# Performance work log

Measured on AMD Instinct MI355X. Metric: run time of the kernel, lower is better.

## Reference

```python
import jax, jax.numpy as jnp
import numpy as np

NUM_HEADS = 8

def _feature_map(t):
    return jax.nn.elu(t) + 1.0

def setup_inputs() -> dict:
    key = jax.random.key(0)
    ks = jax.random.split(key, 7)
    B, S, D = 2, 1024, 512
    sc = 1.0 / np.sqrt(D)
    return {
        'x':  jax.random.normal(ks[0], (B, S, D), dtype=jnp.float32),
        'Wq': jax.random.normal(ks[1], (D, D), dtype=jnp.float32) * sc,
        'Wk': jax.random.normal(ks[2], (D, D), dtype=jnp.float32) * sc,
        'Wv': jax.random.normal(ks[3], (D, D), dtype=jnp.float32) * sc,
        'Wo': jax.random.normal(ks[4], (D, D), dtype=jnp.float32) * sc,
        'bo': jnp.zeros((D,), dtype=jnp.float32),
        'Wg': jax.random.normal(ks[5], (2 * D, D), dtype=jnp.float32) * (1.0 / np.sqrt(2 * D)),
        'bg': jnp.zeros((D,), dtype=jnp.float32),
    }

def reference(x, Wq, Wk, Wv, Wo, bo, Wg, bg):
    B, S, D = x.shape
    H = NUM_HEADS
    hd = D // H
    # projections, split heads -> [B,S,H,hd]
    q = _feature_map((x @ Wq).reshape(B, S, H, hd))
    k = _feature_map((x @ Wk).reshape(B, S, H, hd))
    v = (x @ Wv).reshape(B, S, H, hd)
    # causal linear attention via cumulative sums
    kv = jnp.einsum('bshd,bshe->bshde', k, v)        # [B,S,H,hd,hd]
    kv_cumsum = jnp.cumsum(kv, axis=1)
    k_cumsum = jnp.cumsum(k, axis=1)
    numerator = jnp.einsum('bshd,bshde->bshe', q, kv_cumsum)
    denominator = jnp.einsum('bshd,bshd->bsh', q, k_cumsum)[..., None]
    out = (numerator / (denominator + 1e-6)).reshape(B, S, D)
    out = out @ Wo + bo
    gate = jax.nn.sigmoid(jnp.concatenate([x, out], axis=-1) @ Wg + bg)
    return x + gate * (out - x)
```

## Files before the change

### kernel.cpp

```cpp
#include <hip/hip_runtime.h>
#include <hip/hip_bf16.h>
#include <math.h>


typedef __bf16 bf16x8 __attribute__((ext_vector_type(8)));
typedef __bf16 bf16x4 __attribute__((ext_vector_type(4)));
typedef float f32x4 __attribute__((ext_vector_type(4)));

#define MFMA16(a, b, c) __builtin_amdgcn_mfma_f32_16x16x32_bf16(a, b, c, 0, 0, 0)

__device__ __forceinline__ float elu1(float v) { return v > 0.f ? v + 1.f : __expf(v); }

__device__ __forceinline__ void gload16(const void* g, void* l) {
    __builtin_amdgcn_global_load_lds((const __attribute__((address_space(1))) void*)g,
                                     (__attribute__((address_space(3))) void*)l, 16, 0, 0);
}

__global__ __launch_bounds__(256) void prep_kernel(
    const float* __restrict__ x, const float* __restrict__ Wq, const float* __restrict__ Wk,
    const float* __restrict__ Wv, const float* __restrict__ Wo, const float* __restrict__ Wg,
    __bf16* __restrict__ xb, __bf16* __restrict__ wqkvT, __bf16* __restrict__ woT,
    __bf16* __restrict__ wgT) {
    int z = blockIdx.z;
    if (z == 5) {
        int bid = blockIdx.y * 16 + blockIdx.x;
        int base = (bid * 256 + threadIdx.x) * 8;
        bf16x8 o;
#pragma unroll
        for (int j = 0; j < 8; j++) o[j] = (__bf16)x[base + j];
        *(bf16x8*)&xb[base] = o;
        return;
    }
    const float* in;
    __bf16* out;
    int R = 512, C = 512;
    if (z == 0) { in = Wq; out = wqkvT; }
    else if (z == 1) { in = Wk; out = wqkvT + (size_t)512 * 512; }
    else if (z == 2) { in = Wv; out = wqkvT + (size_t)1024 * 512; }
    else if (z == 3) { in = Wo; out = woT; }
    else { in = Wg; out = wgT; R = 1024; }
    if ((int)blockIdx.y * 32 >= R) return;
    __shared__ float t[32][33];
    int bx = blockIdx.x, by = blockIdx.y;
    int tx = threadIdx.x & 31, ty = threadIdx.x >> 5;
#pragma unroll
    for (int i = 0; i < 32; i += 8)
        t[ty + i][tx] = in[(size_t)(by * 32 + ty + i) * C + bx * 32 + tx];
    __syncthreads();
#pragma unroll
    for (int i = 0; i < 32; i += 8)
        out[(size_t)(bx * 32 + ty + i) * R + by * 32 + tx] = (__bf16)t[tx][ty + i];
}

template <int MODE, int BM, int BN>
__global__ __launch_bounds__(256) void gemm_kernel(
    const __bf16* __restrict__ A, const __bf16* __restrict__ A2,
    const __bf16* __restrict__ Bw, const float* __restrict__ bias,
    const float* __restrict__ xf, const float* __restrict__ proj,
    float* __restrict__ outf, __bf16* __restrict__ outb,
    __bf16* __restrict__ q_out, __bf16* __restrict__ k_out,
    __bf16* __restrict__ kt_out, __bf16* __restrict__ vt_out, int K) {
    constexpr int MI = BM / 32, NI = BN / 32;
    constexpr int LA = BM / 64, LB = BN / 64;
    constexpr int L = LA + LB;
    __shared__ __bf16 sA[3 * BM * 32];
    __shared__ __bf16 sB[3 * BN * 32];
    int bm = blockIdx.x, bn = blockIdx.y;
    int tid = threadIdx.x, w = tid >> 6, l = tid & 63;
    int wr = (w >> 1) * (16 * MI), wc = (w & 1) * (16 * NI);
    int r = tid >> 2, c = (tid & 3) * 8;
    f32x4 acc[MI][NI] = {};
    const int nt = K / 32;

    auto stage = [&](int t, int buf) {
        int k0 = t * 32;
        const __bf16* a0 = A;
        int gka = k0, lda = K;
        if (MODE == 2) {
            lda = 512;
            if (k0 >= 512) { a0 = A2; gka = k0 - 512; }
        }
#pragma unroll
        for (int i = 0; i < LA; i++)
            gload16(&a0[(size_t)(bm * BM + i * 64 + r) * lda + gka + c],
                    &sA[buf * (BM * 32) + i * 2048 + w * 512]);
#pragma unroll
        for (int i = 0; i < LB; i++)
            gload16(&Bw[(size_t)(bn * BN + i * 64 + r) * K + k0 + c],
                    &sB[buf * (BN * 32) + i * 2048 + w * 512]);
    };

    stage(0, 0);
    stage(1, 1);
    for (int t = 0; t < nt; t++) {
        if (t + 1 < nt) {
            if constexpr (L == 2) asm volatile("s_waitcnt vmcnt(2)" ::: "memory");
            else asm volatile("s_waitcnt vmcnt(3)" ::: "memory");
        } else {
            asm volatile("s_waitcnt vmcnt(0)" ::: "memory");
        }
        asm volatile("s_barrier" ::: "memory");
        if (t + 2 < nt) stage(t + 2, (t + 2) % 3);
        int buf = t % 3;
        bf16x8 af[MI], bfr[NI];
#pragma unroll
        for (int mi = 0; mi < MI; mi++)
            af[mi] = *(const bf16x8*)&sA[buf * (BM * 32) + (wr + mi * 16 + (l & 15)) * 32 + ((l >> 4) << 3)];
#pragma unroll
        for (int ni = 0; ni < NI; ni++)
            bfr[ni] = *(const bf16x8*)&sB[buf * (BN * 32) + (wc + ni * 16 + (l & 15)) * 32 + ((l >> 4) << 3)];
#pragma unroll
        for (int mi = 0; mi < MI; mi++)
#pragma unroll
            for (int ni = 0; ni < NI; ni++)
                acc[mi][ni] = MFMA16(af[mi], bfr[ni], acc[mi][ni]);
    }

    if (MODE == 0) {
#pragma unroll
        for (int mi = 0; mi < MI; mi++) {
            int gm0 = bm * BM + wr + mi * 16 + ((l >> 4) << 2);
            int b = gm0 >> 10, s0 = gm0 & 1023;
#pragma unroll
            for (int ni = 0; ni < NI; ni++) {
                int gn = bn * BN + wc + ni * 16 + (l & 15);
                int which = gn >> 9, h = (gn >> 6) & 7, d = gn & 63;
                int bh = b * 8 + h;
                if (which == 0) {
#pragma unroll
                    for (int j = 0; j < 4; j++)
                        q_out[((size_t)(bh * 1024 + s0 + j)) * 64 + d] = (__bf16)elu1(acc[mi][ni][j]);
                } else if (which == 1) {
                    bf16x4 pk;
#pragma unroll
                    for (int j = 0; j < 4; j++) {
                        __bf16 tb = (__bf16)elu1(acc[mi][ni][j]);
                        pk[j] = tb;
                        k_out[((size_t)(bh * 1024 + s0 + j)) * 64 + d] = tb;
                    }
                    *(bf16x4*)&kt_out[((size_t)(bh * 64 + d)) * 1024 + s0] = pk;
                } else {
                    bf16x4 pv;
#pragma unroll
                    for (int j = 0; j < 4; j++) pv[j] = (__bf16)acc[mi][ni][j];
                    *(bf16x4*)&vt_out[((size_t)(bh * 64 + d)) * 1024 + s0] = pv;
                }
            }
        }
    } else {
#pragma unroll
        for (int mi = 0; mi < MI; mi++)
#pragma unroll
            for (int ni = 0; ni < NI; ni++)
#pragma unroll
                for (int j = 0; j < 4; j++) {
                    int gm = bm * BM + wr + mi * 16 + ((l >> 4) << 2) + j;
                    int gn = bn * BN + wc + ni * 16 + (l & 15);
                    float v = acc[mi][ni][j] + bias[gn];
                    if (MODE == 1) {
                        outf[(size_t)gm * 512 + gn] = v;
                        outb[(size_t)gm * 512 + gn] = (__bf16)v;
                    } else {
                        float g = 1.f / (1.f + __expf(-v));
                        float xv = xf[(size_t)gm * 512 + gn];
                        float pv = proj[(size_t)gm * 512 + gn];
                        outf[(size_t)gm * 512 + gn] = xv + g * (pv - xv);
                    }
                }
    }
}

__global__ __launch_bounds__(256) void mc_kernel(const __bf16* __restrict__ ktb,
                                                 const __bf16* __restrict__ vtb,
                                                 float* __restrict__ Mc, float* __restrict__ ksc) {
    int blk = blockIdx.x;
    int bh = blk >> 3, ch = blk & 7;
    int tid = threadIdx.x, w = tid >> 6, l = tid & 63;
    const __bf16* vb = vtb + (size_t)bh * 65536 + ch * 128;
    const __bf16* kp = ktb + (size_t)bh * 65536 + ch * 128;
    f32x4 macc[4] = {};
#pragma unroll
    for (int ks = 0; ks < 4; ks++) {
        bf16x8 a = *(const bf16x8*)&vb[(size_t)(w * 16 + (l & 15)) * 1024 + ks * 32 + ((l >> 4) << 3)];
#pragma unroll
        for (int ni = 0; ni < 4; ni++) {
            bf16x8 bb = *(const bf16x8*)&kp[(size_t)(ni * 16 + (l & 15)) * 1024 + ks * 32 + ((l >> 4) << 3)];
            macc[ni] = MFMA16(a, bb, macc[ni]);
        }
    }
    float* mout = Mc + (size_t)blk * 4096;
#pragma unroll
    for (int ni = 0; ni < 4; ni++)
#pragma unroll
        for (int j = 0; j < 4; j++)
            mout[(size_t)(w * 16 + ((l >> 4) << 2) + j) * 64 + ni * 16 + (l & 15)] = macc[ni][j];
    if (tid < 64) {
        float s = 0.f;
        const __bf16* kr = ktb + (size_t)(bh * 64 + tid) * 1024 + ch * 128;
#pragma unroll
        for (int t = 0; t < 16; t++) {
            bf16x8 v = *(const bf16x8*)&kr[t * 8];
#pragma unroll
            for (int j = 0; j < 8; j++) s += (float)v[j];
        }
        ksc[blk * 64 + tid] = s;
    }
}

__global__ __launch_bounds__(256) void attn_chunk_kernel(
    const __bf16* __restrict__ qb, const __bf16* __restrict__ kb,
    const __bf16* __restrict__ vtb, const float* __restrict__ Mc,
    const float* __restrict__ ksc, __bf16* __restrict__ attn_out) {
    int blk = blockIdx.x;
    int bh = blk >> 3, ch = blk & 7;
    int b = bh >> 3, h = bh & 7;
    int tid = threadIdx.x, w = tid >> 6, l = tid & 63;

    __shared__ __bf16 sQ[128 * 72];
    __shared__ __bf16 sP[128 * 136];
    __shared__ __bf16 sM[64 * 72];
    __shared__ float den2[128];
    __shared__ float dpart[2][128];
    __shared__ float ksst[64];

    const __bf16* qsrc = qb + (size_t)(bh * 1024 + ch * 128) * 64;
#pragma unroll
    for (int i = 0; i < 4; i++) {
        int e = i * 2048 + tid * 8;
        *(bf16x8*)&sQ[(e >> 6) * 72 + (e & 63)] = *(const bf16x8*)&qsrc[e];
    }
    {
        int r0 = tid >> 2;
        int c0 = (tid & 3) * 16;
        f32x4 s0 = {}, s1 = {}, s2 = {}, s3 = {};
        const float* mcb = Mc + (size_t)(bh * 8) * 4096 + r0 * 64 + c0;
        for (int c = 0; c < ch; c++) {
            const float* p = mcb + (size_t)c * 4096;
            s0 += *(const f32x4*)&p[0];
            s1 += *(const f32x4*)&p[4];
            s2 += *(const f32x4*)&p[8];
            s3 += *(const f32x4*)&p[12];
        }
        __bf16* d = &sM[r0 * 72 + c0];
#pragma unroll
        for (int j = 0; j < 4; j++) {
            d[j] = (__bf16)s0[j];
            d[4 + j] = (__bf16)s1[j];
            d[8 + j] = (__bf16)s2[j];
            d[12 + j] = (__bf16)s3[j];
        }
    }
    if (tid < 64) {
        float s = 0.f;
        for (int c = 0; c < ch; c++) s += ksc[(bh * 8 + c) * 64 + tid];
        ksst[tid] = s;
    }
    __syncthreads();

    if (w == 1) {
#pragma unroll
        for (int rr = 0; rr < 2; rr++) {
            int row = rr * 64 + l;
            float s = 0.f;
#pragma unroll
            for (int d0 = 0; d0 < 64; d0 += 8) {
                bf16x8 qv = *(const bf16x8*)&sQ[row * 72 + d0];
#pragma unroll
                for (int jj = 0; jj < 8; jj++) s += (float)qv[jj] * ksst[d0 + jj];
            }
            den2[row] = s;
        }
        dpart[1][l] = 0.f;
    } else {
        int wr = (w == 0) ? 0 : 64;
        int wc = (w == 3) ? 64 : 0;
        const bool diag = (w != 2);
        f32x4 acc[4][4] = {};
        const __bf16* kbase = kb + (size_t)(bh * 1024 + ch * 128) * 64;
#pragma unroll
        for (int ks = 0; ks < 2; ks++) {
            bf16x8 a[4], bfr[4];
#pragma unroll
            for (int mi = 0; mi < 4; mi++)
                a[mi] = *(const bf16x8*)&sQ[(wr + mi * 16 + (l & 15)) * 72 + ks * 32 + ((l >> 4) << 3)];
#pragma unroll
            for (int ni = 0; ni < 4; ni++)
                bfr[ni] = *(const bf16x8*)&kbase[(size_t)(wc + ni * 16 + (l & 15)) * 64 + ks * 32 + ((l >> 4) << 3)];
#pragma unroll
            for (int mi = 0; mi < 4; mi++)
#pragma unroll
                for (int ni = 0; ni < 4; ni++)
                    acc[mi][ni] = MFMA16(a[mi], bfr[ni], acc[mi][ni]);
        }
        int dp = (w == 3) ? 1 : 0;
#pragma unroll
        for (int mi = 0; mi < 4; mi++) {
#pragma unroll
            for (int j = 0; j < 4; j++) {
                int row = wr + mi * 16 + ((l >> 4) << 2) + j;
                float rs = 0.f;
#pragma unroll
                for (int ni = 0; ni < 4; ni++) {
                    int col = wc + ni * 16 + (l & 15);
                    float v = acc[mi][ni][j];
                    if (diag) v = (col <= row) ? v : 0.f;
                    rs += v;
                    sP[row * 136 + col] = (__bf16)v;
                }
#pragma unroll
                for (int off = 1; off < 16; off <<= 1) rs += __shfl_xor(rs, off);
                if ((l & 15) == 0) dpart[dp][row] = rs;
            }
        }
    }
    __syncthreads();

    f32x4 o[2][4] = {};
    const __bf16* vbase = vtb + (size_t)bh * 65536 + ch * 128;
    for (int ks = 0; ks <= w; ks++) {
        bf16x8 a[2], bfr[4];
#pragma unroll
        for (int mi = 0; mi < 2; mi++)
            a[mi] = *(const bf16x8*)&sP[(w * 32 + mi * 16 + (l & 15)) * 136 + ks * 32 + ((l >> 4) << 3)];
#pragma unroll
        for (int ni = 0; ni < 4; ni++)
            bfr[ni] = *(const bf16x8*)&vbase[(size_t)(ni * 16 + (l & 15)) * 1024 + ks * 32 + ((l >> 4) << 3)];
#pragma unroll
        for (int mi = 0; mi < 2; mi++)
#pragma unroll
            for (int ni = 0; ni < 4; ni++)
                o[mi][ni] = MFMA16(a[mi], bfr[ni], o[mi][ni]);
    }
    if (ch > 0) {
#pragma unroll
        for (int ks = 0; ks < 2; ks++) {
            bf16x8 a[2], bfr[4];
#pragma unroll
            for (int mi = 0; mi < 2; mi++)
                a[mi] = *(const bf16x8*)&sQ[(w * 32 + mi * 16 + (l & 15)) * 72 + ks * 32 + ((l >> 4) << 3)];
#pragma unroll
            for (int ni = 0; ni < 4; ni++)
                bfr[ni] = *(const bf16x8*)&sM[(ni * 16 + (l & 15)) * 72 + ks * 32 + ((l >> 4) << 3)];
#pragma unroll
            for (int mi = 0; mi < 2; mi++)
#pragma unroll
                for (int ni = 0; ni < 4; ni++)
                    o[mi][ni] = MFMA16(a[mi], bfr[ni], o[mi][ni]);
        }
    }

    __bf16* obase = attn_out + ((size_t)(b * 1024 + ch * 128)) * 512 + h * 64;
#pragma unroll
    for (int mi = 0; mi < 2; mi++)
#pragma unroll
        for (int j = 0; j < 4; j++) {
            int row = w * 32 + mi * 16 + ((l >> 4) << 2) + j;
            float dn = den2[row] + dpart[0][row] + dpart[1][row] + 1e-6f;
#pragma unroll
            for (int ni = 0; ni < 4; ni++) {
                int col = ni * 16 + (l & 15);
                obase[(size_t)row * 512 + col] = (__bf16)(o[mi][ni][j] / dn);
            }
        }
}

extern "C" void kernel_launch(void* const* d_in, const int* in_sizes, int n_in,
                              void* d_out, int out_size, void* d_ws, size_t ws_size,
                              hipStream_t stream) {
    const float* x = (const float*)d_in[0];
    const float* Wq = (const float*)d_in[1];
    const float* Wk = (const float*)d_in[2];
    const float* Wv = (const float*)d_in[3];
    const float* Wo = (const float*)d_in[4];
    const float* bo = (const float*)d_in[5];
    const float* Wg = (const float*)d_in[6];
    const float* bg = (const float*)d_in[7];
    float* out = (float*)d_out;

    char* ws = (char*)d_ws;
    size_t off = 0;
    auto alloc = [&](size_t bytes) -> void* {
        void* p = ws + off;
        off += (bytes + 255) & ~(size_t)255;
        return p;
    };
    __bf16* xb    = (__bf16*)alloc((size_t)2048 * 512 * 2);
    __bf16* wqkvT = (__bf16*)alloc((size_t)1536 * 512 * 2);
    __bf16* woT   = (__bf16*)alloc((size_t)512 * 512 * 2);
    __bf16* wgT   = (__bf16*)alloc((size_t)512 * 1024 * 2);
    __bf16* qb    = (__bf16*)alloc((size_t)16 * 1024 * 64 * 2);
    __bf16* kb    = (__bf16*)alloc((size_t)16 * 1024 * 64 * 2);
    __bf16* ktb   = (__bf16*)alloc((size_t)16 * 64 * 1024 * 2);
    __bf16* vtb   = (__bf16*)alloc((size_t)16 * 64 * 1024 * 2);
    float*  Mc    = (float*)alloc((size_t)128 * 4096 * 4);
    float*  ksc   = (float*)alloc((size_t)128 * 64 * 4);
    __bf16* attn  = (__bf16*)alloc((size_t)2048 * 512 * 2);
    float*  proj  = (float*)alloc((size_t)2048 * 512 * 4);
    __bf16* projb = (__bf16*)alloc((size_t)2048 * 512 * 2);

    prep_kernel<<<dim3(16, 32, 6), 256, 0, stream>>>(x, Wq, Wk, Wv, Wo, Wg, xb, wqkvT, woT, wgT);
    gemm_kernel<0, 64, 128><<<dim3(32, 12), 256, 0, stream>>>(
        xb, nullptr, wqkvT, nullptr, nullptr, nullptr, nullptr, nullptr, qb, kb, ktb, vtb, 512);
    mc_kernel<<<128, 256, 0, stream>>>(ktb, vtb, Mc, ksc);
    attn_chunk_kernel<<<128, 256, 0, stream>>>(qb, kb, vtb, Mc, ksc, attn);
    gemm_kernel<1, 64, 64><<<dim3(32, 8), 256, 0, stream>>>(
        attn, nullptr, woT, bo, nullptr, nullptr, proj, projb, nullptr, nullptr, nullptr, nullptr, 512);
    gemm_kernel<2, 64, 64><<<dim3(32, 8), 256, 0, stream>>>(
        xb, projb, wgT, bg, x, proj, out, nullptr, nullptr, nullptr, nullptr, nullptr, 1024);
}
```

Before: 65.71 us.

## Fold x·Wg into QKV GEMM, fuse out-proj with gate, split attention chunks

Appends the x-half of the gate weight to the fused QKV weight, so the QKV GEMM also writes the x·Wg partial in fp32. The separate output-projection and gate GEMMs are merged into one kernel that keeps the projected rows in LDS and applies bias, sigmoid and blend directly. The attention kernel is split into half-chunks with 256 blocks and skips causally masked tiles. This removes two launches and the proj/projb round trips through global memory and improves attention occupancy. The cost is that projgate uses only 128 blocks, with each block reading all of Wo and Wg2 from global memory without LDS staging.

```diff
diff --git a/kernel.cpp b/kernel.cpp
--- a/kernel.cpp
+++ b/kernel.cpp
@@ -19,8 +19,8 @@
 __global__ __launch_bounds__(256) void prep_kernel(
     const float* __restrict__ x, const float* __restrict__ Wq, const float* __restrict__ Wk,
     const float* __restrict__ Wv, const float* __restrict__ Wo, const float* __restrict__ Wg,
-    __bf16* __restrict__ xb, __bf16* __restrict__ wqkvT, __bf16* __restrict__ woT,
-    __bf16* __restrict__ wgT) {
+    __bf16* __restrict__ xb, __bf16* __restrict__ wqkvgT, __bf16* __restrict__ woT,
+    __bf16* __restrict__ wg2T) {
     int z = blockIdx.z;
     if (z == 5) {
         int bid = blockIdx.y * 16 + blockIdx.x;
@@ -32,83 +32,73 @@
         return;
     }
     const float* in;
-    __bf16* out;
-    int R = 512, C = 512;
-    if (z == 0) { in = Wq; out = wqkvT; }
-    else if (z == 1) { in = Wk; out = wqkvT + (size_t)512 * 512; }
-    else if (z == 2) { in = Wv; out = wqkvT + (size_t)1024 * 512; }
-    else if (z == 3) { in = Wo; out = woT; }
-    else { in = Wg; out = wgT; R = 1024; }
+    int R = 512;
+    if (z == 0) in = Wq;
+    else if (z == 1) in = Wk;
+    else if (z == 2) in = Wv;
+    else if (z == 3) in = Wo;
+    else { in = Wg; R = 1024; }
     if ((int)blockIdx.y * 32 >= R) return;
     __shared__ float t[32][33];
     int bx = blockIdx.x, by = blockIdx.y;
     int tx = threadIdx.x & 31, ty = threadIdx.x >> 5;
 #pragma unroll
     for (int i = 0; i < 32; i += 8)
-        t[ty + i][tx] = in[(size_t)(by * 32 + ty + i) * C + bx * 32 + tx];
+        t[ty + i][tx] = in[(size_t)(by * 32 + ty + i) * 512 + bx * 32 + tx];
     __syncthreads();
 #pragma unroll
-    for (int i = 0; i < 32; i += 8)
-        out[(size_t)(bx * 32 + ty + i) * R + by * 32 + tx] = (__bf16)t[tx][ty + i];
-}
-
-template <int MODE, int BM, int BN>
-__global__ __launch_bounds__(256) void gemm_kernel(
-    const __bf16* __restrict__ A, const __bf16* __restrict__ A2,
-    const __bf16* __restrict__ Bw, const float* __restrict__ bias,
-    const float* __restrict__ xf, const float* __restrict__ proj,
-    float* __restrict__ outf, __bf16* __restrict__ outb,
+    for (int i = 0; i < 32; i += 8) {
+        int n = bx * 32 + ty + i;
+        int kk = by * 32 + tx;
+        __bf16 val = (__bf16)t[tx][ty + i];
+        if (z == 0) wqkvgT[(size_t)n * 512 + kk] = val;
+        else if (z == 1) wqkvgT[(size_t)(512 + n) * 512 + kk] = val;
+        else if (z == 2) wqkvgT[(size_t)(1024 + n) * 512 + kk] = val;
+        else if (z == 3) woT[(size_t)n * 512 + kk] = val;
+        else if (kk < 512) wqkvgT[(size_t)(1536 + n) * 512 + kk] = val;
+        else wg2T[(size_t)n * 512 + (kk - 512)] = val;
+    }
+}
+
+__global__ __launch_bounds__(256) void qkv_kernel(
+    const __bf16* __restrict__ A, const __bf16* __restrict__ Bw,
     __bf16* __restrict__ q_out, __bf16* __restrict__ k_out,
-    __bf16* __restrict__ kt_out, __bf16* __restrict__ vt_out, int K) {
-    constexpr int MI = BM / 32, NI = BN / 32;
-    constexpr int LA = BM / 64, LB = BN / 64;
-    constexpr int L = LA + LB;
+    __bf16* __restrict__ kt_out, __bf16* __restrict__ vt_out, float* __restrict__ xg) {
+    constexpr int BM = 64, BN = 128;
+    constexpr int MI = 2, NI = 4;
     __shared__ __bf16 sA[3 * BM * 32];
     __shared__ __bf16 sB[3 * BN * 32];
     int bm = blockIdx.x, bn = blockIdx.y;
     int tid = threadIdx.x, w = tid >> 6, l = tid & 63;
-    int wr = (w >> 1) * (16 * MI), wc = (w & 1) * (16 * NI);
+    int wr = (w >> 1) * 32, wc = (w & 1) * 64;
     int r = tid >> 2, c = (tid & 3) * 8;
     f32x4 acc[MI][NI] = {};
-    const int nt = K / 32;
+    const int nt = 16;
 
     auto stage = [&](int t, int buf) {
         int k0 = t * 32;
-        const __bf16* a0 = A;
-        int gka = k0, lda = K;
-        if (MODE == 2) {
-            lda = 512;
-            if (k0 >= 512) { a0 = A2; gka = k0 - 512; }
-        }
-#pragma unroll
-        for (int i = 0; i < LA; i++)
-            gload16(&a0[(size_t)(bm * BM + i * 64 + r) * lda + gka + c],
-                    &sA[buf * (BM * 32) + i * 2048 + w * 512]);
-#pragma unroll
-        for (int i = 0; i < LB; i++)
-            gload16(&Bw[(size_t)(bn * BN + i * 64 + r) * K + k0 + c],
-                    &sB[buf * (BN * 32) + i * 2048 + w * 512]);
+        gload16(&A[(size_t)(bm * BM + r) * 512 + k0 + c], &sA[buf * 2048 + w * 512]);
+#pragma unroll
+        for (int i = 0; i < 2; i++)
+            gload16(&Bw[(size_t)(bn * BN + i * 64 + r) * 512 + k0 + c],
+                    &sB[buf * 4096 + i * 2048 + w * 512]);
     };
 
     stage(0, 0);
     stage(1, 1);
     for (int t = 0; t < nt; t++) {
-        if (t + 1 < nt) {
-            if constexpr (L == 2) asm volatile("s_waitcnt vmcnt(2)" ::: "memory");
-            else asm volatile("s_waitcnt vmcnt(3)" ::: "memory");
-        } else {
-            asm volatile("s_waitcnt vmcnt(0)" ::: "memory");
-        }
+        if (t + 1 < nt) asm volatile("s_waitcnt vmcnt(3)" ::: "memory");
+        else asm volatile("s_waitcnt vmcnt(0)" ::: "memory");
         asm volatile("s_barrier" ::: "memory");
         if (t + 2 < nt) stage(t + 2, (t + 2) % 3);
         int buf = t % 3;
         bf16x8 af[MI], bfr[NI];
 #pragma unroll
         for (int mi = 0; mi < MI; mi++)
-            af[mi] = *(const bf16x8*)&sA[buf * (BM * 32) + (wr + mi * 16 + (l & 15)) * 32 + ((l >> 4) << 3)];
+            af[mi] = *(const bf16x8*)&sA[buf * 2048 + (wr + mi * 16 + (l & 15)) * 32 + ((l >> 4) << 3)];
 #pragma unroll
         for (int ni = 0; ni < NI; ni++)
-            bfr[ni] = *(const bf16x8*)&sB[buf * (BN * 32) + (wc + ni * 16 + (l & 15)) * 32 + ((l >> 4) << 3)];
+            bfr[ni] = *(const bf16x8*)&sB[buf * 4096 + (wc + ni * 16 + (l & 15)) * 32 + ((l >> 4) << 3)];
 #pragma unroll
         for (int mi = 0; mi < MI; mi++)
 #pragma unroll
@@ -116,57 +106,39 @@
                 acc[mi][ni] = MFMA16(af[mi], bfr[ni], acc[mi][ni]);
     }
 
-    if (MODE == 0) {
-#pragma unroll
-        for (int mi = 0; mi < MI; mi++) {
-            int gm0 = bm * BM + wr + mi * 16 + ((l >> 4) << 2);
-            int b = gm0 >> 10, s0 = gm0 & 1023;
-#pragma unroll
-            for (int ni = 0; ni < NI; ni++) {
-                int gn = bn * BN + wc + ni * 16 + (l & 15);
-                int which = gn >> 9, h = (gn >> 6) & 7, d = gn & 63;
-                int bh = b * 8 + h;
-                if (which == 0) {
-#pragma unroll
-                    for (int j = 0; j < 4; j++)
-                        q_out[((size_t)(bh * 1024 + s0 + j)) * 64 + d] = (__bf16)elu1(acc[mi][ni][j]);
-                } else if (which == 1) {
-                    bf16x4 pk;
-#pragma unroll
-                    for (int j = 0; j < 4; j++) {
-                        __bf16 tb = (__bf16)elu1(acc[mi][ni][j]);
-                        pk[j] = tb;
-                        k_out[((size_t)(bh * 1024 + s0 + j)) * 64 + d] = tb;
-                    }
-                    *(bf16x4*)&kt_out[((size_t)(bh * 64 + d)) * 1024 + s0] = pk;
-                } else {
-                    bf16x4 pv;
-#pragma unroll
-                    for (int j = 0; j < 4; j++) pv[j] = (__bf16)acc[mi][ni][j];
-                    *(bf16x4*)&vt_out[((size_t)(bh * 64 + d)) * 1024 + s0] = pv;
+#pragma unroll
+    for (int mi = 0; mi < MI; mi++) {
+        int gm0 = bm * BM + wr + mi * 16 + ((l >> 4) << 2);
+        int b = gm0 >> 10, s0 = gm0 & 1023;
+#pragma unroll
+        for (int ni = 0; ni < NI; ni++) {
+            int gn = bn * BN + wc + ni * 16 + (l & 15);
+            int which = gn >> 9, h = (gn >> 6) & 7, d = gn & 63;
+            int bh = b * 8 + h;
+            if (which == 0) {
+#pragma unroll
+                for (int j = 0; j < 4; j++)
+                    q_out[((size_t)(bh * 1024 + s0 + j)) * 64 + d] = (__bf16)elu1(acc[mi][ni][j]);
+            } else if (which == 1) {
+                bf16x4 pk;
+#pragma unroll
+                for (int j = 0; j < 4; j++) {
+                    __bf16 tb = (__bf16)elu1(acc[mi][ni][j]);
+                    pk[j] = tb;
+                    k_out[((size_t)(bh * 1024 + s0 + j)) * 64 + d] = tb;
                 }
-            }
-        }
-    } else {
-#pragma unroll
-        for (int mi = 0; mi < MI; mi++)
-#pragma unroll
-            for (int ni = 0; ni < NI; ni++)
-#pragma unroll
-                for (int j = 0; j < 4; j++) {
-                    int gm = bm * BM + wr + mi * 16 + ((l >> 4) << 2) + j;
-                    int gn = bn * BN + wc + ni * 16 + (l & 15);
-                    float v = acc[mi][ni][j] + bias[gn];
-                    if (MODE == 1) {
-                        outf[(size_t)gm * 512 + gn] = v;
-                        outb[(size_t)gm * 512 + gn] = (__bf16)v;
-                    } else {
-                        float g = 1.f / (1.f + __expf(-v));
-                        float xv = xf[(size_t)gm * 512 + gn];
-                        float pv = proj[(size_t)gm * 512 + gn];
-                        outf[(size_t)gm * 512 + gn] = xv + g * (pv - xv);
-                    }
-                }
+                *(bf16x4*)&kt_out[((size_t)(bh * 64 + d)) * 1024 + s0] = pk;
+            } else if (which == 2) {
+                bf16x4 pv;
+#pragma unroll
+                for (int j = 0; j < 4; j++) pv[j] = (__bf16)acc[mi][ni][j];
+                *(bf16x4*)&vt_out[((size_t)(bh * 64 + d)) * 1024 + s0] = pv;
+            } else {
+#pragma unroll
+                for (int j = 0; j < 4; j++)
+                    xg[(size_t)(gm0 + j) * 512 + (gn & 511)] = acc[mi][ni][j];
+            }
+        }
     }
 }
 
@@ -207,31 +179,30 @@
     }
 }
 
-__global__ __launch_bounds__(256) void attn_chunk_kernel(
+__global__ __launch_bounds__(256) void attn_kernel(
     const __bf16* __restrict__ qb, const __bf16* __restrict__ kb,
     const __bf16* __restrict__ vtb, const float* __restrict__ Mc,
     const float* __restrict__ ksc, __bf16* __restrict__ attn_out) {
     int blk = blockIdx.x;
-    int bh = blk >> 3, ch = blk & 7;
+    int bh = blk >> 4, ch = (blk >> 1) & 7, half = blk & 1;
     int b = bh >> 3, h = bh & 7;
     int tid = threadIdx.x, w = tid >> 6, l = tid & 63;
 
-    __shared__ __bf16 sQ[128 * 72];
-    __shared__ __bf16 sP[128 * 136];
+    __shared__ __bf16 sQ[64 * 72];
+    __shared__ __bf16 sP[64 * 136];
     __shared__ __bf16 sM[64 * 72];
-    __shared__ float den2[128];
-    __shared__ float dpart[2][128];
+    __shared__ float den[64];
+    __shared__ float rsum[64];
     __shared__ float ksst[64];
 
-    const __bf16* qsrc = qb + (size_t)(bh * 1024 + ch * 128) * 64;
-#pragma unroll
-    for (int i = 0; i < 4; i++) {
+    const __bf16* qsrc = qb + (size_t)(bh * 1024 + ch * 128 + half * 64) * 64;
+#pragma unroll
+    for (int i = 0; i < 2; i++) {
         int e = i * 2048 + tid * 8;
         *(bf16x8*)&sQ[(e >> 6) * 72 + (e & 63)] = *(const bf16x8*)&qsrc[e];
     }
     {
-        int r0 = tid >> 2;
-        int c0 = (tid & 3) * 16;
+        int r0 = tid >> 2, c0 = (tid & 3) * 16;
         f32x4 s0 = {}, s1 = {}, s2 = {}, s3 = {};
         const float* mcb = Mc + (size_t)(bh * 8) * 4096 + r0 * 64 + c0;
         for (int c = 0; c < ch; c++) {
@@ -257,111 +228,163 @@
     }
     __syncthreads();
 
-    if (w == 1) {
-#pragma unroll
-        for (int rr = 0; rr < 2; rr++) {
-            int row = rr * 64 + l;
-            float s = 0.f;
-#pragma unroll
-            for (int d0 = 0; d0 < 64; d0 += 8) {
-                bf16x8 qv = *(const bf16x8*)&sQ[row * 72 + d0];
-#pragma unroll
-                for (int jj = 0; jj < 8; jj++) s += (float)qv[jj] * ksst[d0 + jj];
-            }
-            den2[row] = s;
-        }
-        dpart[1][l] = 0.f;
-    } else {
-        int wr = (w == 0) ? 0 : 64;
-        int wc = (w == 3) ? 64 : 0;
-        const bool diag = (w != 2);
-        f32x4 acc[4][4] = {};
+    if (tid < 64) {
+        float s = 0.f;
+#pragma unroll
+        for (int d0 = 0; d0 < 64; d0 += 8) {
+            bf16x8 qv = *(const bf16x8*)&sQ[tid * 72 + d0];
+#pragma unroll
+            for (int jj = 0; jj < 8; jj++) s += (float)qv[jj] * ksst[d0 + jj];
+        }
+        den[tid] = s;
+    }
+
+    {
+        int wr = w * 16;
+        const int CFMAX = half ? (w + 4) : w;
+        const int CFLIM = half ? 7 : 3;
         const __bf16* kbase = kb + (size_t)(bh * 1024 + ch * 128) * 64;
-#pragma unroll
-        for (int ks = 0; ks < 2; ks++) {
-            bf16x8 a[4], bfr[4];
-#pragma unroll
-            for (int mi = 0; mi < 4; mi++)
-                a[mi] = *(const bf16x8*)&sQ[(wr + mi * 16 + (l & 15)) * 72 + ks * 32 + ((l >> 4) << 3)];
-#pragma unroll
-            for (int ni = 0; ni < 4; ni++)
-                bfr[ni] = *(const bf16x8*)&kbase[(size_t)(wc + ni * 16 + (l & 15)) * 64 + ks * 32 + ((l >> 4) << 3)];
-#pragma unroll
-            for (int mi = 0; mi < 4; mi++)
-#pragma unroll
-                for (int ni = 0; ni < 4; ni++)
-                    acc[mi][ni] = MFMA16(a[mi], bfr[ni], acc[mi][ni]);
-        }
-        int dp = (w == 3) ? 1 : 0;
-#pragma unroll
-        for (int mi = 0; mi < 4; mi++) {
+        bf16x8 aq[2];
+#pragma unroll
+        for (int ks = 0; ks < 2; ks++)
+            aq[ks] = *(const bf16x8*)&sQ[(wr + (l & 15)) * 72 + ks * 32 + ((l >> 4) << 3)];
+        f32x4 acc[8] = {};
+#pragma unroll
+        for (int cf = 0; cf < 8; cf++) {
+            if (cf <= CFMAX && cf <= CFLIM) {
+#pragma unroll
+                for (int ks = 0; ks < 2; ks++) {
+                    bf16x8 bfr = *(const bf16x8*)&kbase[(size_t)(cf * 16 + (l & 15)) * 64 + ks * 32 + ((l >> 4) << 3)];
+                    acc[cf] = MFMA16(aq[ks], bfr, acc[cf]);
+                }
+            }
+        }
+#pragma unroll
+        for (int j = 0; j < 4; j++) {
+            int lrow = wr + ((l >> 4) << 2) + j;
+            int grow = half * 64 + lrow;
+            float rs = 0.f;
+#pragma unroll
+            for (int cf = 0; cf < 8; cf++) {
+                if (cf <= CFMAX && cf <= CFLIM) {
+                    int col = cf * 16 + (l & 15);
+                    float v = acc[cf][j];
+                    v = (col <= grow) ? v : 0.f;
+                    rs += v;
+                    sP[lrow * 136 + col] = (__bf16)v;
+                }
+            }
+            if (CFMAX + 1 <= CFLIM) sP[lrow * 136 + (CFMAX + 1) * 16 + (l & 15)] = (__bf16)0.f;
+#pragma unroll
+            for (int off = 1; off < 16; off <<= 1) rs += __shfl_xor(rs, off);
+            if ((l & 15) == 0) rsum[lrow] = rs;
+        }
+    }
+    __syncthreads();
+
+    f32x4 o[4] = {};
+    {
+        int wr = w * 16;
+        int ksmax = half ? (2 + (w >> 1)) : (w >> 1);
+        const __bf16* vbase = vtb + (size_t)bh * 65536 + ch * 128;
+#pragma unroll
+        for (int ks = 0; ks < 4; ks++) {
+            if (ks <= ksmax) {
+                bf16x8 a = *(const bf16x8*)&sP[(wr + (l & 15)) * 136 + ks * 32 + ((l >> 4) << 3)];
+#pragma unroll
+                for (int ni = 0; ni < 4; ni++) {
+                    bf16x8 bfr = *(const bf16x8*)&vbase[(size_t)(ni * 16 + (l & 15)) * 1024 + ks * 32 + ((l >> 4) << 3)];
+                    o[ni] = MFMA16(a, bfr, o[ni]);
+                }
+            }
+        }
+        if (ch > 0) {
+#pragma unroll
+            for (int ks = 0; ks < 2; ks++) {
+                bf16x8 a = *(const bf16x8*)&sQ[(wr + (l & 15)) * 72 + ks * 32 + ((l >> 4) << 3)];
+#pragma unroll
+                for (int ni = 0; ni < 4; ni++) {
+                    bf16x8 bfr = *(const bf16x8*)&sM[(ni * 16 + (l & 15)) * 72 + ks * 32 + ((l >> 4) << 3)];
+                    o[ni] = MFMA16(a, bfr, o[ni]);
+                }
+            }
+        }
+    }
+
+    __bf16* obase = attn_out + ((size_t)(b * 1024 + ch * 128 + half * 64)) * 512 + h * 64;
+#pragma unroll
+    for (int j = 0; j < 4; j++) {
+        int lrow = w * 16 + ((l >> 4) << 2) + j;
+        float dn = den[lrow] + rsum[lrow] + 1e-6f;
+#pragma unroll
+        for (int ni = 0; ni < 4; ni++) {
+            int col = ni * 16 + (l & 15);
+            obase[(size_t)lrow * 512 + col] = (__bf16)(o[ni][j] / dn);
+        }
+    }
+}
+
+__global__ __launch_bounds__(256) void projgate_kernel(
+    const __bf16* __restrict__ attn, const __bf16* __restrict__ woT,
+    const __bf16* __restrict__ wg2T, const float* __restrict__ bo,
+    const float* __restrict__ bg, const float* __restrict__ xg,
+    const float* __restrict__ x, float* __restrict__ out) {
+    __shared__ float pPf[16 * 516];
+    int bm = blockIdx.x;
+    int tid = threadIdx.x, w = tid >> 6, l = tid & 63;
+    int gm0 = bm * 16;
+
+    {
+        f32x4 acc[8] = {};
+        const __bf16* abase = attn + (size_t)gm0 * 512;
+#pragma unroll
+        for (int ks = 0; ks < 16; ks++) {
+            bf16x8 a = *(const bf16x8*)&abase[(size_t)(l & 15) * 512 + ks * 32 + ((l >> 4) << 3)];
+#pragma unroll
+            for (int ni = 0; ni < 8; ni++) {
+                bf16x8 bfr = *(const bf16x8*)&woT[(size_t)(w * 128 + ni * 16 + (l & 15)) * 512 + ks * 32 + ((l >> 4) << 3)];
+                acc[ni] = MFMA16(a, bfr, acc[ni]);
+            }
+        }
+#pragma unroll
+        for (int ni = 0; ni < 8; ni++)
 #pragma unroll
             for (int j = 0; j < 4; j++) {
-                int row = wr + mi * 16 + ((l >> 4) << 2) + j;
-                float rs = 0.f;
-#pragma unroll
-                for (int ni = 0; ni < 4; ni++) {
-                    int col = wc + ni * 16 + (l & 15);
-                    float v = acc[mi][ni][j];
-                    if (diag) v = (col <= row) ? v : 0.f;
-                    rs += v;
-                    sP[row * 136 + col] = (__bf16)v;
-                }
-#pragma unroll
-                for (int off = 1; off < 16; off <<= 1) rs += __shfl_xor(rs, off);
-                if ((l & 15) == 0) dpart[dp][row] = rs;
-            }
-        }
+                int row = ((l >> 4) << 2) + j;
+                int col = w * 128 + ni * 16 + (l & 15);
+                pPf[row * 516 + col] = acc[ni][j] + bo[col];
+            }
     }
     __syncthreads();
 
-    f32x4 o[2][4] = {};
-    const __bf16* vbase = vtb + (size_t)bh * 65536 + ch * 128;
-    for (int ks = 0; ks <= w; ks++) {
-        bf16x8 a[2], bfr[4];
-#pragma unroll
-        for (int mi = 0; mi < 2; mi++)
-            a[mi] = *(const bf16x8*)&sP[(w * 32 + mi * 16 + (l & 15)) * 136 + ks * 32 + ((l >> 4) << 3)];
-#pragma unroll
-        for (int ni = 0; ni < 4; ni++)
-            bfr[ni] = *(const bf16x8*)&vbase[(size_t)(ni * 16 + (l & 15)) * 1024 + ks * 32 + ((l >> 4) << 3)];
-#pragma unroll
-        for (int mi = 0; mi < 2; mi++)
-#pragma unroll
-            for (int ni = 0; ni < 4; ni++)
-                o[mi][ni] = MFMA16(a[mi], bfr[ni], o[mi][ni]);
-    }
-    if (ch > 0) {
-#pragma unroll
-        for (int ks = 0; ks < 2; ks++) {
-            bf16x8 a[2], bfr[4];
-#pragma unroll
-            for (int mi = 0; mi < 2; mi++)
-                a[mi] = *(const bf16x8*)&sQ[(w * 32 + mi * 16 + (l & 15)) * 72 + ks * 32 + ((l >> 4) << 3)];
-#pragma unroll
-            for (int ni = 0; ni < 4; ni++)
-                bfr[ni] = *(const bf16x8*)&sM[(ni * 16 + (l & 15)) * 72 + ks * 32 + ((l >> 4) << 3)];
-#pragma unroll
-            for (int mi = 0; mi < 2; mi++)
-#pragma unroll
-                for (int ni = 0; ni < 4; ni++)
-                    o[mi][ni] = MFMA16(a[mi], bfr[ni], o[mi][ni]);
-        }
-    }
-
-    __bf16* obase = attn_out + ((size_t)(b * 1024 + ch * 128)) * 512 + h * 64;
-#pragma unroll
-    for (int mi = 0; mi < 2; mi++)
-#pragma unroll
-        for (int j = 0; j < 4; j++) {
-            int row = w * 32 + mi * 16 + ((l >> 4) << 2) + j;
-            float dn = den2[row] + dpart[0][row] + dpart[1][row] + 1e-6f;
-#pragma unroll
-            for (int ni = 0; ni < 4; ni++) {
-                int col = ni * 16 + (l & 15);
-                obase[(size_t)row * 512 + col] = (__bf16)(o[mi][ni][j] / dn);
-            }
-        }
+    {
+        f32x4 acc[8] = {};
+#pragma unroll
+        for (int ks = 0; ks < 16; ks++) {
+            const float* pr = &pPf[(l & 15) * 516 + ks * 32 + ((l >> 4) << 3)];
+            bf16x8 a;
+#pragma unroll
+            for (int j = 0; j < 8; j++) a[j] = (__bf16)pr[j];
+#pragma unroll
+            for (int ni = 0; ni < 8; ni++) {
+                bf16x8 bfr = *(const bf16x8*)&wg2T[(size_t)(w * 128 + ni * 16 + (l & 15)) * 512 + ks * 32 + ((l >> 4) << 3)];
+                acc[ni] = MFMA16(a, bfr, acc[ni]);
+            }
+        }
+#pragma unroll
+        for (int ni = 0; ni < 8; ni++)
+#pragma unroll
+            for (int j = 0; j < 4; j++) {
+                int row = ((l >> 4) << 2) + j;
+                int col = w * 128 + ni * 16 + (l & 15);
+                int gm = gm0 + row;
+                float gv = acc[ni][j] + xg[(size_t)gm * 512 + col] + bg[col];
+                float g = 1.f / (1.f + __expf(-gv));
+                float xv = x[(size_t)gm * 512 + col];
+                float pv = pPf[row * 516 + col];
+                out[(size_t)gm * 512 + col] = xv + g * (pv - xv);
+            }
+    }
 }
 
 extern "C" void kernel_launch(void* const* d_in, const int* in_sizes, int n_in,
@@ -384,27 +407,22 @@
         off += (bytes + 255) & ~(size_t)255;
         return p;
     };
-    __bf16* xb    = (__bf16*)alloc((size_t)2048 * 512 * 2);
-    __bf16* wqkvT = (__bf16*)alloc((size_t)1536 * 512 * 2);
-    __bf16* woT   = (__bf16*)alloc((size_t)512 * 512 * 2);
-    __bf16* wgT   = (__bf16*)alloc((size_t)512 * 1024 * 2);
-    __bf16* qb    = (__bf16*)alloc((size_t)16 * 1024 * 64 * 2);
-    __bf16* kb    = (__bf16*)alloc((size_t)16 * 1024 * 64 * 2);
-    __bf16* ktb   = (__bf16*)alloc((size_t)16 * 64 * 1024 * 2);
-    __bf16* vtb   = (__bf16*)alloc((size_t)16 * 64 * 1024 * 2);
-    float*  Mc    = (float*)alloc((size_t)128 * 4096 * 4);
-    float*  ksc   = (float*)alloc((size_t)128 * 64 * 4);
-    __bf16* attn  = (__bf16*)alloc((size_t)2048 * 512 * 2);
-    float*  proj  = (float*)alloc((size_t)2048 * 512 * 4);
-    __bf16* projb = (__bf16*)alloc((size_t)2048 * 512 * 2);
-
-    prep_kernel<<<dim3(16, 32, 6), 256, 0, stream>>>(x, Wq, Wk, Wv, Wo, Wg, xb, wqkvT, woT, wgT);
-    gemm_kernel<0, 64, 128><<<dim3(32, 12), 256, 0, stream>>>(
-        xb, nullptr, wqkvT, nullptr, nullptr, nullptr, nullptr, nullptr, qb, kb, ktb, vtb, 512);
+    __bf16* xb     = (__bf16*)alloc((size_t)2048 * 512 * 2);
+    __bf16* wqkvgT = (__bf16*)alloc((size_t)2048 * 512 * 2);
+    __bf16* woT    = (__bf16*)alloc((size_t)512 * 512 * 2);
+    __bf16* wg2T   = (__bf16*)alloc((size_t)512 * 512 * 2);
+    __bf16* qb     = (__bf16*)alloc((size_t)16 * 1024 * 64 * 2);
+    __bf16* kb     = (__bf16*)alloc((size_t)16 * 1024 * 64 * 2);
+    __bf16* ktb    = (__bf16*)alloc((size_t)16 * 64 * 1024 * 2);
+    __bf16* vtb    = (__bf16*)alloc((size_t)16 * 64 * 1024 * 2);
+    float*  Mc     = (float*)alloc((size_t)128 * 4096 * 4);
+    float*  ksc    = (float*)alloc((size_t)128 * 64 * 4);
+    __bf16* attn   = (__bf16*)alloc((size_t)2048 * 512 * 2);
+    float*  xg     = (float*)alloc((size_t)2048 * 512 * 4);
+
+    prep_kernel<<<dim3(16, 32, 6), 256, 0, stream>>>(x, Wq, Wk, Wv, Wo, Wg, xb, wqkvgT, woT, wg2T);
+    qkv_kernel<<<dim3(32, 16), 256, 0, stream>>>(xb, wqkvgT, qb, kb, ktb, vtb, xg);
     mc_kernel<<<128, 256, 0, stream>>>(ktb, vtb, Mc, ksc);
-    attn_chunk_kernel<<<128, 256, 0, stream>>>(qb, kb, vtb, Mc, ksc, attn);
-    gemm_kernel<1, 64, 64><<<dim3(32, 8), 256, 0, stream>>>(
-        attn, nullptr, woT, bo, nullptr, nullptr, proj, projb, nullptr, nullptr, nullptr, nullptr, 512);
-    gemm_kernel<2, 64, 64><<<dim3(32, 8), 256, 0, stream>>>(
-        xb, projb, wgT, bg, x, proj, out, nullptr, nullptr, nullptr, nullptr, nullptr, 1024);
-}
+    attn_kernel<<<256, 256, 0, stream>>>(qb, kb, vtb, Mc, ksc, attn);
+    projgate_kernel<<<128, 256, 0, stream>>>(attn, woT, wg2T, bo, bg, xg, x, out);
+}
```

Result: slower. 76.55 us (+16.5%).

## Split attention chunks into row halves and deepen GEMM pipeline to four stages

Applied to the files above, without the earlier changes.

The attention kernel now launches two blocks per 128-row chunk, each handling 64 query rows. Each wave computes its 16-row QK^T strip and skips the causally masked column tiles. Work across waves is more balanced and twice as many blocks are available to fill the GPU, at the cost of duplicated Mc prefix sums and K/V loads per half. Separately, the GEMM prefetch goes from 3 to 4 LDS buffers with adjusted vmcnt waits, hiding more load latency while using more shared memory.

```diff
diff --git a/kernel.cpp b/kernel.cpp
--- a/kernel.cpp
+++ b/kernel.cpp
@@ -63,8 +63,8 @@
     constexpr int MI = BM / 32, NI = BN / 32;
     constexpr int LA = BM / 64, LB = BN / 64;
     constexpr int L = LA + LB;
-    __shared__ __bf16 sA[3 * BM * 32];
-    __shared__ __bf16 sB[3 * BN * 32];
+    __shared__ __bf16 sA[4 * BM * 32];
+    __shared__ __bf16 sB[4 * BN * 32];
     int bm = blockIdx.x, bn = blockIdx.y;
     int tid = threadIdx.x, w = tid >> 6, l = tid & 63;
     int wr = (w >> 1) * (16 * MI), wc = (w & 1) * (16 * NI);
@@ -92,16 +92,20 @@
 
     stage(0, 0);
     stage(1, 1);
+    stage(2, 2);
     for (int t = 0; t < nt; t++) {
-        if (t + 1 < nt) {
+        if (t + 2 < nt) {
+            if constexpr (L == 2) asm volatile("s_waitcnt vmcnt(4)" ::: "memory");
+            else asm volatile("s_waitcnt vmcnt(6)" ::: "memory");
+        } else if (t + 1 < nt) {
             if constexpr (L == 2) asm volatile("s_waitcnt vmcnt(2)" ::: "memory");
             else asm volatile("s_waitcnt vmcnt(3)" ::: "memory");
         } else {
             asm volatile("s_waitcnt vmcnt(0)" ::: "memory");
         }
         asm volatile("s_barrier" ::: "memory");
-        if (t + 2 < nt) stage(t + 2, (t + 2) % 3);
-        int buf = t % 3;
+        if (t + 3 < nt) stage(t + 3, (t + 3) & 3);
+        int buf = t & 3;
         bf16x8 af[MI], bfr[NI];
 #pragma unroll
         for (int mi = 0; mi < MI; mi++)
@@ -207,31 +211,30 @@
     }
 }
 
-__global__ __launch_bounds__(256) void attn_chunk_kernel(
+__global__ __launch_bounds__(256) void attn_kernel(
     const __bf16* __restrict__ qb, const __bf16* __restrict__ kb,
     const __bf16* __restrict__ vtb, const float* __restrict__ Mc,
     const float* __restrict__ ksc, __bf16* __restrict__ attn_out) {
     int blk = blockIdx.x;
-    int bh = blk >> 3, ch = blk & 7;
+    int bh = blk >> 4, ch = (blk >> 1) & 7, half = blk & 1;
     int b = bh >> 3, h = bh & 7;
     int tid = threadIdx.x, w = tid >> 6, l = tid & 63;
 
-    __shared__ __bf16 sQ[128 * 72];
-    __shared__ __bf16 sP[128 * 136];
+    __shared__ __bf16 sQ[64 * 72];
+    __shared__ __bf16 sP[64 * 136];
     __shared__ __bf16 sM[64 * 72];
-    __shared__ float den2[128];
-    __shared__ float dpart[2][128];
+    __shared__ float den[64];
+    __shared__ float rsum[64];
     __shared__ float ksst[64];
 
-    const __bf16* qsrc = qb + (size_t)(bh * 1024 + ch * 128) * 64;
-#pragma unroll
-    for (int i = 0; i < 4; i++) {
+    const __bf16* qsrc = qb + (size_t)(bh * 1024 + ch * 128 + half * 64) * 64;
+#pragma unroll
+    for (int i = 0; i < 2; i++) {
         int e = i * 2048 + tid * 8;
         *(bf16x8*)&sQ[(e >> 6) * 72 + (e & 63)] = *(const bf16x8*)&qsrc[e];
     }
     {
-        int r0 = tid >> 2;
-        int c0 = (tid & 3) * 16;
+        int r0 = tid >> 2, c0 = (tid & 3) * 16;
         f32x4 s0 = {}, s1 = {}, s2 = {}, s3 = {};
         const float* mcb = Mc + (size_t)(bh * 8) * 4096 + r0 * 64 + c0;
         for (int c = 0; c < ch; c++) {
@@ -257,111 +260,100 @@
     }
     __syncthreads();
 
-    if (w == 1) {
-#pragma unroll
-        for (int rr = 0; rr < 2; rr++) {
-            int row = rr * 64 + l;
-            float s = 0.f;
-#pragma unroll
-            for (int d0 = 0; d0 < 64; d0 += 8) {
-                bf16x8 qv = *(const bf16x8*)&sQ[row * 72 + d0];
-#pragma unroll
-                for (int jj = 0; jj < 8; jj++) s += (float)qv[jj] * ksst[d0 + jj];
+    if (tid < 64) {
+        float s = 0.f;
+#pragma unroll
+        for (int d0 = 0; d0 < 64; d0 += 8) {
+            bf16x8 qv = *(const bf16x8*)&sQ[tid * 72 + d0];
+#pragma unroll
+            for (int jj = 0; jj < 8; jj++) s += (float)qv[jj] * ksst[d0 + jj];
+        }
+        den[tid] = s;
+    }
+
+    {
+        int wr = w * 16;
+        const int CFMAX = half ? (w + 4) : w;
+        const int CFLIM = half ? 7 : 3;
+        const __bf16* kbase = kb + (size_t)(bh * 1024 + ch * 128) * 64;
+        bf16x8 aq[2];
+#pragma unroll
+        for (int ks = 0; ks < 2; ks++)
+            aq[ks] = *(const bf16x8*)&sQ[(wr + (l & 15)) * 72 + ks * 32 + ((l >> 4) << 3)];
+        f32x4 acc[8] = {};
+#pragma unroll
+        for (int cf = 0; cf < 8; cf++) {
+            if (cf <= CFMAX && cf <= CFLIM) {
+#pragma unroll
+                for (int ks = 0; ks < 2; ks++) {
+                    bf16x8 bfr = *(const bf16x8*)&kbase[(size_t)(cf * 16 + (l & 15)) * 64 + ks * 32 + ((l >> 4) << 3)];
+                    acc[cf] = MFMA16(aq[ks], bfr, acc[cf]);
+                }
             }
-            den2[row] = s;
-        }
-        dpart[1][l] = 0.f;
-    } else {
-        int wr = (w == 0) ? 0 : 64;
-        int wc = (w == 3) ? 64 : 0;
-        const bool diag = (w != 2);
-        f32x4 acc[4][4] = {};
-        const __bf16* kbase = kb + (size_t)(bh * 1024 + ch * 128) * 64;
-#pragma unroll
-        for (int ks = 0; ks < 2; ks++) {
-            bf16x8 a[4], bfr[4];
-#pragma unroll
-            for (int mi = 0; mi < 4; mi++)
-                a[mi] = *(const bf16x8*)&sQ[(wr + mi * 16 + (l & 15)) * 72 + ks * 32 + ((l >> 4) << 3)];
-#pragma unroll
-            for (int ni = 0; ni < 4; ni++)
-                bfr[ni] = *(const bf16x8*)&kbase[(size_t)(wc + ni * 16 + (l & 15)) * 64 + ks * 32 + ((l >> 4) << 3)];
-#pragma unroll
-            for (int mi = 0; mi < 4; mi++)
-#pragma unroll
-                for (int ni = 0; ni < 4; ni++)
-                    acc[mi][ni] = MFMA16(a[mi], bfr[ni], acc[mi][ni]);
-        }
-        int dp = (w == 3) ? 1 : 0;
-#pragma unroll
-        for (int mi = 0; mi < 4; mi++) {
-#pragma unroll
-            for (int j = 0; j < 4; j++) {
-                int row = wr + mi * 16 + ((l >> 4) << 2) + j;
-                float rs = 0.f;
+        }
+#pragma unroll
+        for (int j = 0; j < 4; j++) {
+            int lrow = wr + ((l >> 4) << 2) + j;
+            int grow = half * 64 + lrow;
+            float rs = 0.f;
+#pragma unroll
+            for (int cf = 0; cf < 8; cf++) {
+                if (cf <= CFMAX && cf <= CFLIM) {
+                    int col = cf * 16 + (l & 15);
+                    float v = acc[cf][j];
+                    v = (col <= grow) ? v : 0.f;
+                    rs += v;
+                    sP[lrow * 136 + col] = (__bf16)v;
+                }
+            }
+            if (CFMAX + 1 <= CFLIM) sP[lrow * 136 + (CFMAX + 1) * 16 + (l & 15)] = (__bf16)0.f;
+#pragma unroll
+            for (int off = 1; off < 16; off <<= 1) rs += __shfl_xor(rs, off);
+            if ((l & 15) == 0) rsum[lrow] = rs;
+        }
+    }
+    __syncthreads();
+
+    f32x4 o[4] = {};
+    {
+        int wr = w * 16;
+        int ksmax = half ? (2 + (w >> 1)) : (w >> 1);
+        const __bf16* vbase = vtb + (size_t)bh * 65536 + ch * 128;
+#pragma unroll
+        for (int ks = 0; ks < 4; ks++) {
+            if (ks <= ksmax) {
+                bf16x8 a = *(const bf16x8*)&sP[(wr + (l & 15)) * 136 + ks * 32 + ((l >> 4) << 3)];
 #pragma unroll
                 for (int ni = 0; ni < 4; ni++) {
-                    int col = wc + ni * 16 + (l & 15);
-                    float v = acc[mi][ni][j];
-                    if (diag) v = (col <= row) ? v : 0.f;
-                    rs += v;
-                    sP[row * 136 + col] = (__bf16)v;
-                }
-#pragma unroll
-                for (int off = 1; off < 16; off <<= 1) rs += __shfl_xor(rs, off);
-                if ((l & 15) == 0) dpart[dp][row] = rs;
+                    bf16x8 bfr = *(const bf16x8*)&vbase[(size_t)(ni * 16 + (l & 15)) * 1024 + ks * 32 + ((l >> 4) << 3)];
+                    o[ni] = MFMA16(a, bfr, o[ni]);
+                }
             }
         }
-    }
-    __syncthreads();
-
-    f32x4 o[2][4] = {};
-    const __bf16* vbase = vtb + (size_t)bh * 65536 + ch * 128;
-    for (int ks = 0; ks <= w; ks++) {
-        bf16x8 a[2], bfr[4];
-#pragma unroll
-        for (int mi = 0; mi < 2; mi++)
-            a[mi] = *(const bf16x8*)&sP[(w * 32 + mi * 16 + (l & 15)) * 136 + ks * 32 + ((l >> 4) << 3)];
-#pragma unroll
-        for (int ni = 0; ni < 4; ni++)
-            bfr[ni] = *(const bf16x8*)&vbase[(size_t)(ni * 16 + (l & 15)) * 1024 + ks * 32 + ((l >> 4) << 3)];
-#pragma unroll
-        for (int mi = 0; mi < 2; mi++)
-#pragma unroll
-            for (int ni = 0; ni < 4; ni++)
-                o[mi][ni] = MFMA16(a[mi], bfr[ni], o[mi][ni]);
-    }
-    if (ch > 0) {
-#pragma unroll
-        for (int ks = 0; ks < 2; ks++) {
-            bf16x8 a[2], bfr[4];
-#pragma unroll
-            for (int mi = 0; mi < 2; mi++)
-                a[mi] = *(const bf16x8*)&sQ[(w * 32 + mi * 16 + (l & 15)) * 72 + ks * 32 + ((l >> 4) << 3)];
-#pragma unroll
-            for (int ni = 0; ni < 4; ni++)
-                bfr[ni] = *(const bf16x8*)&sM[(ni * 16 + (l & 15)) * 72 + ks * 32 + ((l >> 4) << 3)];
-#pragma unroll
-            for (int mi = 0; mi < 2; mi++)
-#pragma unroll
-                for (int ni = 0; ni < 4; ni++)
-                    o[mi][ni] = MFMA16(a[mi], bfr[ni], o[mi][ni]);
-        }
-    }
-
-    __bf16* obase = attn_out + ((size_t)(b * 1024 + ch * 128)) * 512 + h * 64;
-#pragma unroll
-    for (int mi = 0; mi < 2; mi++)
-#pragma unroll
-        for (int j = 0; j < 4; j++) {
-            int row = w * 32 + mi * 16 + ((l >> 4) << 2) + j;
-            float dn = den2[row] + dpart[0][row] + dpart[1][row] + 1e-6f;
-#pragma unroll
-            for (int ni = 0; ni < 4; ni++) {
-                int col = ni * 16 + (l & 15);
-                obase[(size_t)row * 512 + col] = (__bf16)(o[mi][ni][j] / dn);
+        if (ch > 0) {
+#pragma unroll
+            for (int ks = 0; ks < 2; ks++) {
+                bf16x8 a = *(const bf16x8*)&sQ[(wr + (l & 15)) * 72 + ks * 32 + ((l >> 4) << 3)];
+#pragma unroll
+                for (int ni = 0; ni < 4; ni++) {
+                    bf16x8 bfr = *(const bf16x8*)&sM[(ni * 16 + (l & 15)) * 72 + ks * 32 + ((l >> 4) << 3)];
+                    o[ni] = MFMA16(a, bfr, o[ni]);
+                }
             }
         }
+    }
+
+    __bf16* obase = attn_out + ((size_t)(b * 1024 + ch * 128 + half * 64)) * 512 + h * 64;
+#pragma unroll
+    for (int j = 0; j < 4; j++) {
+        int lrow = w * 16 + ((l >> 4) << 2) + j;
+        float dn = den[lrow] + rsum[lrow] + 1e-6f;
+#pragma unroll
+        for (int ni = 0; ni < 4; ni++) {
+            int col = ni * 16 + (l & 15);
+            obase[(size_t)lrow * 512 + col] = (__bf16)(o[ni][j] / dn);
+        }
+    }
 }
 
 extern "C" void kernel_launch(void* const* d_in, const int* in_sizes, int n_in,
@@ -402,7 +394,7 @@
     gemm_kernel<0, 64, 128><<<dim3(32, 12), 256, 0, stream>>>(
         xb, nullptr, wqkvT, nullptr, nullptr, nullptr, nullptr, nullptr, qb, kb, ktb, vtb, 512);
     mc_kernel<<<128, 256, 0, stream>>>(ktb, vtb, Mc, ksc);
-    attn_chunk_kernel<<<128, 256, 0, stream>>>(qb, kb, vtb, Mc, ksc, attn);
+    attn_kernel<<<256, 256, 0, stream>>>(qb, kb, vtb, Mc, ksc, attn);
     gemm_kernel<1, 64, 64><<<dim3(32, 8), 256, 0, stream>>>(
         attn, nullptr, woT, bo, nullptr, nullptr, proj, projb, nullptr, nullptr, nullptr, nullptr, 512);
     gemm_kernel<2, 64, 64><<<dim3(32, 8), 256, 0, stream>>>(
```

Result: no change. 65.06 us (-1.0%).
